# Performance work log

Measured on AMD Instinct MI355X. Metric: run time of the kernel, lower is better.

The kernel has to match this reference:

```python
import jax, jax.numpy as jnp
import numpy as np

T, B = 512, 128
INPUT_SIZE = 512
H = 256
L = 3
NDIR = 2


def setup_inputs() -> dict:
    key = jax.random.key(0)
    ks = jax.random.split(key, 6)
    x = jax.random.normal(ks[0], (T, B, INPUT_SIZE), dtype=jnp.float32)
    h0 = jax.random.normal(ks[1], (L * NDIR, B, H), dtype=jnp.float32)
    # Stacked params: layer 0 input dim == INPUT_SIZE == 2*H == later layer input dims.
    scale_ih = 1.0 / np.sqrt(INPUT_SIZE)
    scale_hh = 1.0 / np.sqrt(H)
    w_ih = jax.random.normal(ks[2], (L, NDIR, 3 * H, INPUT_SIZE), dtype=jnp.float32) * scale_ih
    w_hh = jax.random.normal(ks[3], (L, NDIR, 3 * H, H), dtype=jnp.float32) * scale_hh
    b_ih = jnp.zeros((L, NDIR, 3 * H), dtype=jnp.float32)
    b_hh = jnp.zeros((L, NDIR, 3 * H), dtype=jnp.float32)
    return {"x": x, "h0": h0, "w_ih": w_ih, "w_hh": w_hh, "b_ih": b_ih, "b_hh": b_hh}


def _gru_direction(seq, h0_dir, w_ih, w_hh, b_ih, b_hh, reverse):
    # seq: [T, B, D]; precompute input gates for all steps in one GEMM.
    gate_x = jnp.einsum('tbd,gd->tbg', seq, w_ih) + b_ih  # [T, B, 3H]
    if reverse:
        gate_x = jnp.flip(gate_x, axis=0)

    def step(h_prev, gx):
        gh = h_prev @ w_hh.T + b_hh  # [B, 3H]
        i_r, i_z, i_n = jnp.split(gx, 3, axis=-1)
        h_r, h_z, h_n = jnp.split(gh, 3, axis=-1)
        r = jax.nn.sigmoid(i_r + h_r)
        z = jax.nn.sigmoid(i_z + h_z)
        n = jnp.tanh(i_n + r * h_n)
        h_new = (1.0 - z) * n + z * h_prev
        return h_new, h_new

    h_last, outs = jax.lax.scan(step, h0_dir, gate_x)
    if reverse:
        outs = jnp.flip(outs, axis=0)
    return outs, h_last


def reference(x, h0, w_ih, w_hh, b_ih, b_hh):
    layer_input = x
    h_n = []
    for layer in range(L):
        out_f, h_f = _gru_direction(layer_input, h0[layer * NDIR + 0],
                                    w_ih[layer, 0], w_hh[layer, 0],
                                    b_ih[layer, 0], b_hh[layer, 0], reverse=False)
        out_b, h_b = _gru_direction(layer_input, h0[layer * NDIR + 1],
                                    w_ih[layer, 1], w_hh[layer, 1],
                                    b_ih[layer, 1], b_hh[layer, 1], reverse=True)
        layer_input = jnp.concatenate([out_f, out_b], axis=2)  # [T, B, 2H]
        h_n.append(h_f)
        h_n.append(h_b)
    return jnp.stack(h_n, axis=0)  # [L*2, B, H]
```

## Files before the change

kernel.cpp:

```cpp
#include <hip/hip_runtime.h>
#include <stdint.h>

#define T_LEN 512
#define BATCH 128
#define HID 256
#define MROWS (T_LEN*BATCH)
#define KIN 512

typedef __attribute__((ext_vector_type(8))) short short8;
typedef __attribute__((ext_vector_type(4))) float f32x4;
typedef __attribute__((ext_vector_type(4))) unsigned short u16x4;

static __device__ __forceinline__ float bf2f(unsigned short u) {
  union { unsigned int u; float f; } c; c.u = ((unsigned int)u) << 16; return c.f;
}
static __device__ __forceinline__ unsigned short f2bf(float f) {
  union { float f; unsigned int u; } c; c.f = f;
  unsigned int x = c.u;
  x += 0x7fffu + ((x >> 16) & 1u);
  return (unsigned short)(x >> 16);
}
static __device__ __forceinline__ void gload_lds16(const void* g, void* l) {
  __builtin_amdgcn_global_load_lds((const __attribute__((address_space(1))) unsigned int*)g,
                                   (__attribute__((address_space(3))) unsigned int*)l,
                                   16, 0, 0);
}
static __device__ __forceinline__ float fast_sigm(float x) {
  return __builtin_amdgcn_rcpf(1.0f + __expf(-x));
}
static __device__ __forceinline__ float fast_tanh(float x) {
  float e = __expf(2.0f * x);
  return 1.0f - 2.0f * __builtin_amdgcn_rcpf(1.0f + e);
}

#define MFMA_AG(D, W, B) \
  asm("v_mfma_f32_16x16x32_bf16 %0, %1, %2, %0" : "+v"(D) : "a"(W), "v"(B))
#define MFMA_VG(D, W, B) \
  asm("v_mfma_f32_16x16x32_bf16 %0, %1, %2, %0" : "+v"(D) : "v"(W), "v"(B))

__global__ void cvt_bf16(const float* __restrict__ in, unsigned short* __restrict__ out, long n) {
  long i = ((long)blockIdx.x * blockDim.x + threadIdx.x) * 4;
  const long stride = (long)gridDim.x * blockDim.x * 4;
  for (; i < n; i += stride) {
    f32x4 v = *(const f32x4*)(in + i);
    u16x4 o;
    o[0] = f2bf(v[0]); o[1] = f2bf(v[1]); o[2] = f2bf(v[2]); o[3] = f2bf(v[3]);
    *(u16x4*)(out + i) = o;
  }
}

__global__ __launch_bounds__(256) void gemm_gx(
    const unsigned short* __restrict__ A,
    const unsigned short* __restrict__ Bw,
    const float* __restrict__ bih,
    const float* __restrict__ bhh,
    unsigned short* __restrict__ gx)
{
  __shared__ unsigned short As[128*64];
  __shared__ unsigned short Bs[128*64];
  const int tid = threadIdx.x, lane = tid & 63, wv = tid >> 6;
  const int bid = blockIdx.x;
  const int nt = bid % 12; const long mt = bid / 12;
  const long m0 = mt * 128; const int n0 = nt * 128;
  const int wm = wv >> 1, wn = wv & 1;
  const int r8 = lane >> 3, c8 = lane & 7;

  f32x4 acc[4][4];
  #pragma unroll
  for (int i = 0; i < 4; ++i) {
    #pragma unroll
    for (int j = 0; j < 4; ++j) acc[i][j] = (f32x4)0.0f;
  }

  for (int kt = 0; kt < 8; ++kt) {
    const int kb = kt * 64;
    #pragma unroll
    for (int c = 0; c < 4; ++c) {
      const int rr = c*32 + wv*8;
      gload_lds16(A  + (m0 + rr + r8) * (long)KIN + kb + c8*8, &As[rr*64]);
      gload_lds16(Bw + (long)(n0 + rr + r8) * KIN + kb + c8*8, &Bs[rr*64]);
    }
    __syncthreads();
    #pragma unroll
    for (int kk = 0; kk < 2; ++kk) {
      short8 af[4], bfr[4];
      #pragma unroll
      for (int i = 0; i < 4; ++i)
        af[i] = *(const short8*)&As[(wm*64 + i*16 + (lane&15))*64 + kk*32 + (lane>>4)*8];
      #pragma unroll
      for (int j = 0; j < 4; ++j)
        bfr[j] = *(const short8*)&Bs[(wn*64 + j*16 + (lane&15))*64 + kk*32 + (lane>>4)*8];
      #pragma unroll
      for (int i = 0; i < 4; ++i) {
        #pragma unroll
        for (int j = 0; j < 4; ++j)
          acc[i][j] = __builtin_amdgcn_mfma_f32_16x16x32_bf16(af[i], bfr[j], acc[i][j], 0, 0, 0);
      }
    }
    __syncthreads();
  }

  const int d = (n0 >= 768) ? 1 : 0;
  #pragma unroll
  for (int j = 0; j < 4; ++j) {
    const int n = n0 + wn*64 + j*16 + (lane & 15);
    const int g = n - d*768;
    const float bias = bih[n] + ((g < 512) ? bhh[n] : 0.0f);
    #pragma unroll
    for (int i = 0; i < 4; ++i) {
      const long row = m0 + wm*64 + i*16 + (lane >> 4)*4;
      unsigned short* op = gx + ((long)d*MROWS + row)*768 + g;
      #pragma unroll
      for (int r = 0; r < 4; ++r)
        op[(long)r*768] = f2bf(acc[i][j][r] + bias);
    }
  }
}

__global__ __launch_bounds__(256, 1) void gru_rec(
    const unsigned short* __restrict__ gx,
    const unsigned short* __restrict__ Whh,
    const float* __restrict__ bhh,
    const float* __restrict__ h0,
    unsigned short* __restrict__ act,
    float* __restrict__ hOut,
    const int layer)
{
  __shared__ unsigned short hbuf[2][4096];
  __shared__ float bnl[256];
  const int tid = threadIdx.x, lane = tid & 63, wv = tid >> 6;
  const int d = blockIdx.x >> 3, s = blockIdx.x & 7;
  const int g4 = lane >> 4, c = lane & 15;
  const int mb = s*16 + c;

  short8 aA[8][8];
  short8 aV[4][8];
  {
    const unsigned short* wb = Whh + (long)d*768*256;
    #pragma unroll
    for (int rt = 0; rt < 8; ++rt) {
      const int row = (rt>>2)*256 + wv*64 + (rt&3)*16 + c;
      #pragma unroll
      for (int kf = 0; kf < 8; ++kf)
        aA[rt][kf] = *(const short8*)&wb[row*256 + kf*32 + g4*8];
    }
    #pragma unroll
    for (int jt = 0; jt < 4; ++jt) {
      const int row = 512 + wv*64 + jt*16 + c;
      #pragma unroll
      for (int kf = 0; kf < 8; ++kf)
        aV[jt][kf] = *(const short8*)&wb[row*256 + kf*32 + g4*8];
    }
  }

  bnl[tid] = bhh[d*768 + 512 + tid];

  int woff[4];
  #pragma unroll
  for (int jt = 0; jt < 4; ++jt)
    woff[jt] = (wv*8 + jt*2 + (g4>>1))*128 + c*8 + (g4&1)*4;

  {
    const float* hp = h0 + ((long)(layer*2 + d)*BATCH + mb)*HID + wv*64 + g4*4;
    #pragma unroll
    for (int jt = 0; jt < 4; ++jt) {
      u16x4 hv;
      #pragma unroll
      for (int i = 0; i < 4; ++i) hv[i] = f2bf(hp[jt*16 + i]);
      *(u16x4*)&hbuf[0][woff[jt]] = hv;
    }
  }

  const long t0 = d ? 511 : 0;
  const long dgx = d ? -(long)(BATCH*768) : (long)(BATCH*768);
  const long dac = d ? -(long)(BATCH*512) : (long)(BATCH*512);
  const unsigned short* pg = gx + ((long)d*MROWS + t0*BATCH + mb)*768 + wv*64 + g4*4;
  unsigned short* pa = act + (t0*BATCH + mb)*512 + d*256 + wv*64 + g4*4;

  u16x4 cxA[3][4], cxB[3][4];
  #pragma unroll
  for (int gt = 0; gt < 3; ++gt)
    #pragma unroll
    for (int jt = 0; jt < 4; ++jt)
      cxA[gt][jt] = *(const u16x4*)(pg + gt*256 + jt*16);
  pg += dgx;

  __syncthreads();

#define STEP(P, CX, NX)                                                       \
  {                                                                           \
    _Pragma("unroll") for (int gt = 0; gt < 3; ++gt)                          \
      _Pragma("unroll") for (int jt = 0; jt < 4; ++jt)                        \
        NX[gt][jt] = *(const u16x4*)(pg + gt*256 + jt*16);                    \
    f32x4 acc[12];                                                            \
    _Pragma("unroll") for (int rt = 0; rt < 8; ++rt) acc[rt] = (f32x4)0.0f;   \
    _Pragma("unroll") for (int jt = 0; jt < 4; ++jt)                          \
      acc[8+jt] = *(const f32x4*)&bnl[wv*64 + jt*16 + g4*4];                  \
    _Pragma("unroll") for (int kf = 0; kf < 8; ++kf) {                        \
      short8 b = *(const short8*)&hbuf[P][(kf*64 + lane)*8];                  \
      _Pragma("unroll") for (int rt = 0; rt < 8; ++rt)                        \
        MFMA_AG(acc[rt], aA[rt][kf], b);                                      \
      _Pragma("unroll") for (int jt = 0; jt < 4; ++jt)                        \
        MFMA_VG(acc[8+jt], aV[jt][kf], b);                                    \
    }                                                                         \
    _Pragma("unroll") for (int jt = 0; jt < 4; ++jt) {                        \
      u16x4 hold = *(const u16x4*)&hbuf[P][woff[jt]];                         \
      u16x4 hn;                                                               \
      _Pragma("unroll") for (int i = 0; i < 4; ++i) {                         \
        const float r = fast_sigm(bf2f(CX[0][jt][i]) + acc[jt][i]);           \
        const float z = fast_sigm(bf2f(CX[1][jt][i]) + acc[4+jt][i]);         \
        const float nn = fast_tanh(bf2f(CX[2][jt][i]) + r * acc[8+jt][i]);    \
        const float hf = nn + z * (bf2f(hold[i]) - nn);                       \
        hn[i] = f2bf(hf);                                                     \
      }                                                                       \
      *(u16x4*)&hbuf[P^1][woff[jt]] = hn;                                     \
      *(u16x4*)(pa + jt*16) = hn;                                             \
    }                                                                         \
    pg += dgx; pa += dac;                                                     \
    asm volatile("s_waitcnt lgkmcnt(0)\n\ts_barrier" ::: "memory");           \
  }

  #pragma unroll 1
  for (int t2 = 0; t2 < 256; ++t2) {
    STEP(0, cxA, cxB)
    STEP(1, cxB, cxA)
  }
#undef STEP

  {
    float* po = hOut + ((long)(layer*2 + d)*BATCH + mb)*HID + wv*64 + g4*4;
    #pragma unroll
    for (int jt = 0; jt < 4; ++jt) {
      u16x4 hv = *(const u16x4*)&hbuf[0][woff[jt]];
      #pragma unroll
      for (int i = 0; i < 4; ++i) po[jt*16 + i] = bf2f(hv[i]);
    }
  }
}

extern "C" void kernel_launch(void* const* d_in, const int* in_sizes, int n_in,
                              void* d_out, int out_size, void* d_ws, size_t ws_size,
                              hipStream_t stream) {
  const float* x   = (const float*)d_in[0];
  const float* h0  = (const float*)d_in[1];
  const float* wih = (const float*)d_in[2];
  const float* whh = (const float*)d_in[3];
  const float* bih = (const float*)d_in[4];
  const float* bhh = (const float*)d_in[5];
  float* out = (float*)d_out;
  char* ws = (char*)d_ws;
  unsigned short* actA = (unsigned short*)ws;
  unsigned short* actB = (unsigned short*)(ws + 67108864);
  unsigned short* gxb  = (unsigned short*)(ws + 134217728);
  unsigned short* wihb = (unsigned short*)(ws + 335544320);
  unsigned short* whhb = (unsigned short*)(ws + 340262912);
  if (ws_size < 342622208ULL) return;

  hipLaunchKernelGGL(cvt_bf16, dim3(2048), dim3(256), 0, stream, x,   actA, (long)33554432);
  hipLaunchKernelGGL(cvt_bf16, dim3(512),  dim3(256), 0, stream, wih, wihb, (long)2359296);
  hipLaunchKernelGGL(cvt_bf16, dim3(256),  dim3(256), 0, stream, whh, whhb, (long)1179648);

  for (int l = 0; l < 3; ++l) {
    const unsigned short* Ain = (l == 1) ? actB : actA;
    unsigned short* Aout      = (l == 1) ? actA : actB;
    hipLaunchKernelGGL(gemm_gx, dim3(6144), dim3(256), 0, stream,
                       Ain, wihb + (long)l*1536*512, bih + l*1536, bhh + l*1536, gxb);
    hipLaunchKernelGGL(gru_rec, dim3(16), dim3(256), 0, stream,
                       gxb, whhb + (long)l*2*768*256, bhh + l*1536, h0, Aout, out, l);
  }
}
```

Measured before the change: 4.358 ms.

## Prefetch input gate activations into LDS via async global-to-LDS loads

The recurrent kernel now stages the next step's precomputed input-gate values (gx) into a double-buffered LDS area with global_load_lds, using coalesced 16-byte loads per thread, instead of each thread loading scattered u16x4 fragments into registers. This is meant to cut register pressure from the two cx buffers and make the global reads more coalesced. In exchange it adds about 48KB of LDS, extra LDS reads in the gate epilogue, and a vmcnt(0) wait at every step barrier, which could expose global latency on the serial time loop.

```diff
diff --git a/kernel.cpp b/kernel.cpp
--- a/kernel.cpp
+++ b/kernel.cpp
@@ -127,30 +127,30 @@
     const int layer)
 {
   __shared__ unsigned short hbuf[2][4096];
+  __shared__ unsigned short gxl[2][12288];
   __shared__ float bnl[256];
   const int tid = threadIdx.x, lane = tid & 63, wv = tid >> 6;
   const int d = blockIdx.x >> 3, s = blockIdx.x & 7;
   const int g4 = lane >> 4, c = lane & 15;
   const int mb = s*16 + c;
 
+  const unsigned short* wb = Whh + (long)d*768*256;
+
   short8 aA[8][8];
   short8 aV[4][8];
-  {
-    const unsigned short* wb = Whh + (long)d*768*256;
-    #pragma unroll
-    for (int rt = 0; rt < 8; ++rt) {
-      const int row = (rt>>2)*256 + wv*64 + (rt&3)*16 + c;
-      #pragma unroll
-      for (int kf = 0; kf < 8; ++kf)
-        aA[rt][kf] = *(const short8*)&wb[row*256 + kf*32 + g4*8];
-    }
-    #pragma unroll
-    for (int jt = 0; jt < 4; ++jt) {
-      const int row = 512 + wv*64 + jt*16 + c;
-      #pragma unroll
-      for (int kf = 0; kf < 8; ++kf)
-        aV[jt][kf] = *(const short8*)&wb[row*256 + kf*32 + g4*8];
-    }
+  #pragma unroll
+  for (int rt = 0; rt < 8; ++rt) {
+    const int row = (rt>>2)*256 + wv*64 + (rt&3)*16 + c;
+    #pragma unroll
+    for (int kf = 0; kf < 8; ++kf)
+      aA[rt][kf] = *(const short8*)&wb[row*256 + kf*32 + g4*8];
+  }
+  #pragma unroll
+  for (int jt = 0; jt < 4; ++jt) {
+    const int row = 512 + wv*64 + jt*16 + c;
+    #pragma unroll
+    for (int kf = 0; kf < 8; ++kf)
+      aV[jt][kf] = *(const short8*)&wb[row*256 + kf*32 + g4*8];
   }
 
   bnl[tid] = bhh[d*768 + 512 + tid];
@@ -159,6 +159,8 @@
   #pragma unroll
   for (int jt = 0; jt < 4; ++jt)
     woff[jt] = (wv*8 + jt*2 + (g4>>1))*128 + c*8 + (g4&1)*4;
+
+  const int gA = ((wv*8 + (g4>>1))*16 + c)*8 + (g4&1)*4;
 
   {
     const float* hp = h0 + ((long)(layer*2 + d)*BATCH + mb)*HID + wv*64 + g4*4;
@@ -174,56 +176,58 @@
   const long t0 = d ? 511 : 0;
   const long dgx = d ? -(long)(BATCH*768) : (long)(BATCH*768);
   const long dac = d ? -(long)(BATCH*512) : (long)(BATCH*512);
-  const unsigned short* pg = gx + ((long)d*MROWS + t0*BATCH + mb)*768 + wv*64 + g4*4;
+  const unsigned short* sgbase = gx + ((long)d*MROWS + t0*BATCH + s*16 + c)*768 + (wv*4 + g4)*8;
   unsigned short* pa = act + (t0*BATCH + mb)*512 + d*256 + wv*64 + g4*4;
 
-  u16x4 cxA[3][4], cxB[3][4];
-  #pragma unroll
-  for (int gt = 0; gt < 3; ++gt)
-    #pragma unroll
-    for (int jt = 0; jt < 4; ++jt)
-      cxA[gt][jt] = *(const u16x4*)(pg + gt*256 + jt*16);
-  pg += dgx;
+  #pragma unroll
+  for (int k = 0; k < 6; ++k)
+    gload_lds16(sgbase + k*128, &gxl[0][k*2048 + wv*512]);
+  sgbase += dgx;
 
   __syncthreads();
 
-#define STEP(P, CX, NX)                                                       \
+#define STEP(P)                                                               \
   {                                                                           \
-    _Pragma("unroll") for (int gt = 0; gt < 3; ++gt)                          \
-      _Pragma("unroll") for (int jt = 0; jt < 4; ++jt)                        \
-        NX[gt][jt] = *(const u16x4*)(pg + gt*256 + jt*16);                    \
+    _Pragma("unroll") for (int k = 0; k < 6; ++k)                             \
+      gload_lds16(sgbase + k*128, &gxl[(P)^1][k*2048 + wv*512]);              \
+    sgbase += dgx;                                                            \
     f32x4 acc[12];                                                            \
     _Pragma("unroll") for (int rt = 0; rt < 8; ++rt) acc[rt] = (f32x4)0.0f;   \
     _Pragma("unroll") for (int jt = 0; jt < 4; ++jt)                          \
       acc[8+jt] = *(const f32x4*)&bnl[wv*64 + jt*16 + g4*4];                  \
     _Pragma("unroll") for (int kf = 0; kf < 8; ++kf) {                        \
       short8 b = *(const short8*)&hbuf[P][(kf*64 + lane)*8];                  \
-      _Pragma("unroll") for (int rt = 0; rt < 8; ++rt)                        \
-        MFMA_AG(acc[rt], aA[rt][kf], b);                                      \
-      _Pragma("unroll") for (int jt = 0; jt < 4; ++jt)                        \
-        MFMA_VG(acc[8+jt], aV[jt][kf], b);                                    \
+      MFMA_AG(acc[0], aA[0][kf], b); MFMA_AG(acc[1], aA[1][kf], b);           \
+      MFMA_AG(acc[2], aA[2][kf], b); MFMA_AG(acc[3], aA[3][kf], b);           \
+      MFMA_AG(acc[4], aA[4][kf], b); MFMA_AG(acc[5], aA[5][kf], b);           \
+      MFMA_AG(acc[6], aA[6][kf], b); MFMA_AG(acc[7], aA[7][kf], b);           \
+      MFMA_VG(acc[8],  aV[0][kf], b); MFMA_VG(acc[9],  aV[1][kf], b);         \
+      MFMA_VG(acc[10], aV[2][kf], b); MFMA_VG(acc[11], aV[3][kf], b);         \
     }                                                                         \
     _Pragma("unroll") for (int jt = 0; jt < 4; ++jt) {                        \
+      u16x4 xr = *(const u16x4*)&gxl[P][gA + jt*256];                         \
+      u16x4 xz = *(const u16x4*)&gxl[P][gA + jt*256 + 4096];                  \
+      u16x4 xn = *(const u16x4*)&gxl[P][gA + jt*256 + 8192];                  \
       u16x4 hold = *(const u16x4*)&hbuf[P][woff[jt]];                         \
       u16x4 hn;                                                               \
       _Pragma("unroll") for (int i = 0; i < 4; ++i) {                         \
-        const float r = fast_sigm(bf2f(CX[0][jt][i]) + acc[jt][i]);           \
-        const float z = fast_sigm(bf2f(CX[1][jt][i]) + acc[4+jt][i]);         \
-        const float nn = fast_tanh(bf2f(CX[2][jt][i]) + r * acc[8+jt][i]);    \
+        const float r = fast_sigm(bf2f(xr[i]) + acc[jt][i]);                  \
+        const float z = fast_sigm(bf2f(xz[i]) + acc[4+jt][i]);                \
+        const float nn = fast_tanh(bf2f(xn[i]) + r * acc[8+jt][i]);           \
         const float hf = nn + z * (bf2f(hold[i]) - nn);                       \
         hn[i] = f2bf(hf);                                                     \
       }                                                                       \
-      *(u16x4*)&hbuf[P^1][woff[jt]] = hn;                                     \
+      *(u16x4*)&hbuf[(P)^1][woff[jt]] = hn;                                   \
       *(u16x4*)(pa + jt*16) = hn;                                             \
     }                                                                         \
-    pg += dgx; pa += dac;                                                     \
-    asm volatile("s_waitcnt lgkmcnt(0)\n\ts_barrier" ::: "memory");           \
+    pa += dac;                                                                \
+    asm volatile("s_waitcnt vmcnt(0) lgkmcnt(0)\n\ts_barrier" ::: "memory");  \
   }
 
   #pragma unroll 1
   for (int t2 = 0; t2 < 256; ++t2) {
-    STEP(0, cxA, cxB)
-    STEP(1, cxB, cxA)
+    STEP(0)
+    STEP(1)
   }
 #undef STEP
 
```

New measurement: 3.996 ms. 1.09x faster.
